# Optimization experiments

Hardware: AMD Instinct MI355X
Metric: run time of the kernel (lower is better)

The kernel has to match this reference:

```python
import jax, jax.numpy as jnp
import numpy as np

C, M, G = 16, 64, 16            # hidden states, alphabet, n_gen
T, D = 64, 10                   # number of trees, depth (perfect binary)
N1 = 2 ** (D + 1) - 1           # nodes per tree (heap layout)
DIM = T * N1                    # total nodes = 131008
N_LEAVES = T * 2 ** D
_E = [T * 2 ** l for l in range(1, D + 1)]        # edges at each level l
_U = [T * 2 ** (l - 1) for l in range(1, D + 1)]  # unique parents at each level l
_EOFF = [0] + list(np.cumsum(_E))
_UOFF = [0] + list(np.cumsum(_U))


def _tree_structure():
    base = (np.arange(T) * N1)[:, None]
    pas, chs, ups = [], [], []
    for l in range(1, D + 1):
        ch = (np.arange(2 ** l - 1, 2 ** (l + 1) - 1)[None, :] + base).reshape(-1)
        pa = (ch % N1 - 1) // 2 + (ch // N1) * N1   # heap parent, global index
        up = (np.arange(2 ** (l - 1) - 1, 2 ** l - 1)[None, :] + base).reshape(-1)
        pas.append(pa); chs.append(ch); ups.append(up)
    return np.concatenate(pas), np.concatenate(chs), np.concatenate(ups)


def setup_inputs() -> dict:
    key = jax.random.key(0)
    k1, k2, k3, k4 = jax.random.split(key, 4)
    pa, ch, up = _tree_structure()
    leaves = (np.arange(2 ** D - 1, N1)[None, :] + (np.arange(T) * N1)[:, None]).reshape(-1)
    return {
        'x': jax.random.randint(k1, (DIM,), 0, M, dtype=jnp.int32),
        'leaves': jnp.asarray(leaves, jnp.int32),
        'trees_ind': jnp.asarray(np.repeat(np.arange(T), N1), jnp.int32),
        'parents_flat': jnp.asarray(pa, jnp.int32),
        'children_flat': jnp.asarray(ch, jnp.int32),
        'uparents_flat': jnp.asarray(up, jnp.int32),
        'inv_map': jnp.arange(DIM, dtype=jnp.int32),
        'lambda_A': jax.random.uniform(k2, (C, C, G), jnp.float32),
        'lambda_B': jax.random.uniform(k3, (C, M, G), jnp.float32),
        'lambda_Pi': jax.random.uniform(k4, (C, G), jnp.float32),
    }


def reference(x, leaves, trees_ind, parents_flat, children_flat, uparents_flat, inv_map,
              lambda_A, lambda_B, lambda_Pi):
    # softmax-normalized parameters (per generative model g)
    A = jax.nn.softmax(lambda_A, axis=0)    # (C,C,G)  transition, normalized over arrival state
    Bm = jax.nn.softmax(lambda_B, axis=1)   # (C,M,G)  emission over symbols
    Pi = jax.nn.softmax(lambda_Pi, axis=0)  # (C,G)    leaf prior

    beta = jnp.zeros((DIM, C, G), lambda_A.dtype)
    ll = jnp.zeros((DIM, G), lambda_A.dtype)

    # leaves: beta = Pi * B[:, x_leaf]
    b_leaf = jnp.transpose(Bm[:, x[inv_map[leaves]]], (1, 0, 2))  # (L,C,G)
    beta_leaf = Pi[None] * b_leaf
    nu = beta_leaf.sum(axis=1)                                    # (L,G)
    beta = beta.at[leaves].set(beta_leaf / nu[:, None, :])
    ll = ll.at[leaves].set(jnp.log(nu))

    # bottom-up over levels (static loop, D=10 iterations)
    for l in range(D, 0, -1):
        e0, e1 = _EOFF[l - 1], _EOFF[l]
        u0, u1 = _UOFF[l - 1], _UOFF[l]
        pa = parents_flat[e0:e1]
        ch = children_flat[e0:e1]
        up = uparents_flat[u0:u1]
        beta_ch = beta[ch]                                   # (E,C,G) gather
        t_beta_ch = jnp.einsum('ijg,ejg->eig', A, beta_ch)   # sum_j A[i,j,g]*beta_ch[e,j,g]
        t_sum = jax.ops.segment_sum(t_beta_ch, pa, num_segments=DIM)
        cnt = jax.ops.segment_sum(jnp.ones((pa.shape[0],), beta.dtype), pa, num_segments=DIM)
        t_beta_up = t_sum[up] / cnt[up][:, None, None]       # scatter-mean over children
        b_l = jnp.transpose(Bm[:, x[inv_map[up]]], (1, 0, 2))
        beta_l = b_l * t_beta_up
        nu = beta_l.sum(axis=1)
        beta = beta.at[up].set(beta_l / nu[:, None, :])
        ll = ll.at[up].set(jnp.log(nu))

    # per-tree log-likelihood: scatter-sum of node log nu over trees
    return jax.ops.segment_sum(ll, trees_ind, num_segments=T)  # (T,G)
```

## Files before the change

### kernel.cpp

```cpp
#include <hip/hip_runtime.h>


#define C_DIM 16
#define M_DIM 64
#define G_DIM 16
#define T_TREES 64
#define N1 2047
#define NBLOCKS (T_TREES * G_DIM)
#define BTS 20

__device__ __forceinline__ float4 f4add(float4 a, float4 b) {
    return make_float4(a.x + b.x, a.y + b.y, a.z + b.z, a.w + b.w);
}
__device__ __forceinline__ float4 f4mul(float4 a, float4 b) {
    return make_float4(a.x * b.x, a.y * b.y, a.z * b.z, a.w * b.w);
}
__device__ __forceinline__ float4 f4fma(float4 a, float4 b, float4 c) {
    return make_float4(fmaf(a.x, b.x, c.x), fmaf(a.y, b.y, c.y),
                       fmaf(a.z, b.z, c.z), fmaf(a.w, b.w, c.w));
}
__device__ __forceinline__ float hsum4(float4 a) { return a.x + a.y + a.z + a.w; }

__device__ __forceinline__ float matvec_bt(const float* __restrict__ A,
                                           const float* __restrict__ bt,
                                           const float4 sv[4], float4 bp[4])
{
    float nu = 0.f;
    #pragma unroll
    for (int h = 0; h < 2; ++h) {
        #pragma unroll
        for (int q = 2 * h; q < 2 * h + 2; ++q) {
            const float4 b4 = *(const float4*)(bt + 4 * q);
            float tr[4];
            #pragma unroll
            for (int r = 0; r < 4; ++r) {
                const float4* ar = (const float4*)(A + (4 * q + r) * 16);
                float4 m = f4mul(ar[0], sv[0]);
                m = f4fma(ar[1], sv[1], m);
                m = f4fma(ar[2], sv[2], m);
                m = f4fma(ar[3], sv[3], m);
                tr[r] = hsum4(m);
            }
            bp[q] = f4mul(make_float4(tr[0], tr[1], tr[2], tr[3]), b4);
            nu += hsum4(bp[q]);
        }
        __builtin_amdgcn_sched_barrier(0);
    }
    return nu;
}

__global__ __launch_bounds__(256, 1) void htmm_fused(
    const int* __restrict__ x,
    const int* __restrict__ inv_map,
    const float* __restrict__ lA,
    const float* __restrict__ lB,
    const float* __restrict__ lPi,
    float* __restrict__ out)
{
    const int bid = blockIdx.x;
    const int tid = threadIdx.x;
    const int g = bid >> 6;
    const int t = bid & (T_TREES - 1);

    __shared__ __align__(16) unsigned char smem[32768];
    float* const sA   = (float*)(smem);
    float* const sBt  = (float*)(smem + 1024);
    float* const sPB  = (float*)(smem + 6144);
    float* const sLog = (float*)(smem + 11264);
    float* const sPi  = (float*)(smem + 11520);
    float* const buf1 = (float*)(smem + 6144);
    unsigned char* const xs = smem + 14336;
    float* const buf0 = (float*)(smem + 16384);
    float* const wsum = (float*)(smem + 32752);

    {
        const int base = t * N1;
        for (int i = tid; i < N1; i += 256)
            xs[i] = (unsigned char)x[inv_map[base + i]];
    }
    {
        int j = tid >> 4, i = tid & 15;
        float v = lA[(i * C_DIM + j) * G_DIM + g];
        float mx = v;
        #pragma unroll
        for (int m = 1; m < 16; m <<= 1) mx = fmaxf(mx, __shfl_xor(mx, m, 16));
        float e = __expf(v - mx);
        float s = e;
        #pragma unroll
        for (int m = 1; m < 16; m <<= 1) s += __shfl_xor(s, m, 16);
        sA[i * C_DIM + j] = e / s;
    }
    {
        int c = tid >> 4, l16 = tid & 15;
        float e0 = lB[(c * M_DIM + l16 +  0) * G_DIM + g];
        float e1 = lB[(c * M_DIM + l16 + 16) * G_DIM + g];
        float e2 = lB[(c * M_DIM + l16 + 32) * G_DIM + g];
        float e3 = lB[(c * M_DIM + l16 + 48) * G_DIM + g];
        float mx = fmaxf(fmaxf(e0, e1), fmaxf(e2, e3));
        #pragma unroll
        for (int m = 1; m < 16; m <<= 1) mx = fmaxf(mx, __shfl_xor(mx, m, 16));
        e0 = __expf(e0 - mx); e1 = __expf(e1 - mx);
        e2 = __expf(e2 - mx); e3 = __expf(e3 - mx);
        float s = e0 + e1 + e2 + e3;
        #pragma unroll
        for (int m = 1; m < 16; m <<= 1) s += __shfl_xor(s, m, 16);
        float inv = 1.f / s;
        sBt[(l16 +  0) * BTS + c] = e0 * inv;
        sBt[(l16 + 16) * BTS + c] = e1 * inv;
        sBt[(l16 + 32) * BTS + c] = e2 * inv;
        sBt[(l16 + 48) * BTS + c] = e3 * inv;
    }
    if (tid < C_DIM) {
        float v = lPi[tid * G_DIM + g];
        float mx = v;
        #pragma unroll
        for (int m = 1; m < 16; m <<= 1) mx = fmaxf(mx, __shfl_xor(mx, m, 16));
        float e = __expf(v - mx);
        float s = e;
        #pragma unroll
        for (int m = 1; m < 16; m <<= 1) s += __shfl_xor(s, m, 16);
        sPi[tid] = e / s;
    }
    __syncthreads();

    if (tid < M_DIM) {
        const int xv = tid;
        float pb[16]; float nu = 0.f;
        #pragma unroll
        for (int k = 0; k < 16; ++k) {
            pb[k] = sPi[k] * sBt[xv * BTS + k];
            nu += pb[k];
        }
        const float inv = 0.5f / nu;
        #pragma unroll
        for (int k = 0; k < 16; ++k) pb[k] *= inv;
        sLog[xv] = __logf(nu);
        const float4 pv0 = make_float4(pb[0],  pb[1],  pb[2],  pb[3]);
        const float4 pv1 = make_float4(pb[4],  pb[5],  pb[6],  pb[7]);
        const float4 pv2 = make_float4(pb[8],  pb[9],  pb[10], pb[11]);
        const float4 pv3 = make_float4(pb[12], pb[13], pb[14], pb[15]);
        float ta[16];
        #pragma unroll
        for (int i = 0; i < 16; ++i) {
            const float4* ar = (const float4*)(sA + i * 16);
            float4 m = f4mul(ar[0], pv0);
            m = f4fma(ar[1], pv1, m);
            m = f4fma(ar[2], pv2, m);
            m = f4fma(ar[3], pv3, m);
            ta[i] = hsum4(m);
            if ((i & 3) == 3) __builtin_amdgcn_sched_barrier(0);
        }
        #pragma unroll
        for (int q = 0; q < 4; ++q)
            *(float4*)(&sPB[xv * BTS + 4 * q]) =
                make_float4(ta[4*q], ta[4*q+1], ta[4*q+2], ta[4*q+3]);
    }
    __syncthreads();

    float ll = 0.f;

    {
        const int idx = tid;
        const int p8  = 255 + idx;
        const int xl0 = xs[4 * p8 + 3], xr0 = xs[4 * p8 + 4];
        const int xl1 = xs[4 * p8 + 5], xr1 = xs[4 * p8 + 6];
        const int xva = xs[2 * p8 + 1], xvb = xs[2 * p8 + 2];
        const int xv8 = xs[p8];

        const float* tl0 = &sPB[xl0 * BTS];
        const float* tr0 = &sPB[xr0 * BTS];
        const float* tl1 = &sPB[xl1 * BTS];
        const float* tr1 = &sPB[xr1 * BTS];
        const float* bta = &sBt[xva * BTS];
        const float* btb = &sBt[xvb * BTS];

        float4 bpa[4], bpb[4];
        float nua = 0.f, nub = 0.f;
        #pragma unroll
        for (int q = 0; q < 4; ++q) {
            float4 tva = f4add(*(const float4*)(tl0 + 4*q),
                               *(const float4*)(tr0 + 4*q));
            float4 tvb = f4add(*(const float4*)(tl1 + 4*q),
                               *(const float4*)(tr1 + 4*q));
            bpa[q] = f4mul(tva, *(const float4*)(bta + 4*q));
            bpb[q] = f4mul(tvb, *(const float4*)(btb + 4*q));
            nua += hsum4(bpa[q]);
            nub += hsum4(bpb[q]);
        }
        const float ia = 0.5f / nua, ib = 0.5f / nub;
        float4 s8v[4];
        #pragma unroll
        for (int q = 0; q < 4; ++q)
            s8v[q] = f4add(f4mul(bpa[q], make_float4(ia, ia, ia, ia)),
                           f4mul(bpb[q], make_float4(ib, ib, ib, ib)));

        float4 bp[4];
        const float nu8 = matvec_bt(sA, &sBt[xv8 * BTS], s8v, bp);
        ll += sLog[xl0] + sLog[xr0] + sLog[xl1] + sLog[xr1]
            + __logf(nua * nub * nu8);
        const float inv = 1.f / nu8;
        #pragma unroll
        for (int q = 0; q < 4; ++q) {
            buf0[(4*q + 0) * 256 + idx] = bp[q].x * inv;
            buf0[(4*q + 1) * 256 + idx] = bp[q].y * inv;
            buf0[(4*q + 2) * 256 + idx] = bp[q].z * inv;
            buf0[(4*q + 3) * 256 + idx] = bp[q].w * inv;
        }
    }
    __syncthreads();

    if (tid < 128) {
        const int idx = tid;
        float4 sv[4];
        #pragma unroll
        for (int q = 0; q < 4; ++q) {
            float2 c0 = *(const float2*)(&buf0[(4*q + 0) * 256 + 2 * idx]);
            float2 c1 = *(const float2*)(&buf0[(4*q + 1) * 256 + 2 * idx]);
            float2 c2 = *(const float2*)(&buf0[(4*q + 2) * 256 + 2 * idx]);
            float2 c3 = *(const float2*)(&buf0[(4*q + 3) * 256 + 2 * idx]);
            sv[q] = make_float4(0.5f * (c0.x + c0.y), 0.5f * (c1.x + c1.y),
                                0.5f * (c2.x + c2.y), 0.5f * (c3.x + c3.y));
        }
        const int xv = xs[127 + idx];
        float4 bp[4];
        float nu = matvec_bt(sA, &sBt[xv * BTS], sv, bp);
        ll += __logf(nu);
        const float inv = 1.f / nu;
        #pragma unroll
        for (int q = 0; q < 4; ++q) {
            buf1[(4*q + 0) * 128 + idx] = bp[q].x * inv;
            buf1[(4*q + 1) * 128 + idx] = bp[q].y * inv;
            buf1[(4*q + 2) * 128 + idx] = bp[q].z * inv;
            buf1[(4*q + 3) * 128 + idx] = bp[q].w * inv;
        }
    }
    __syncthreads();

    if (tid < 64) {
        float* cur = buf1; int cs = 128;
        float* nxt = buf0; int ns = 256;

        {
            const int idx = tid;
            float4 sv[4];
            #pragma unroll
            for (int q = 0; q < 4; ++q) {
                float2 c0 = *(const float2*)(&cur[(4*q + 0) * cs + 2 * idx]);
                float2 c1 = *(const float2*)(&cur[(4*q + 1) * cs + 2 * idx]);
                float2 c2 = *(const float2*)(&cur[(4*q + 2) * cs + 2 * idx]);
                float2 c3 = *(const float2*)(&cur[(4*q + 3) * cs + 2 * idx]);
                sv[q] = make_float4(0.5f * (c0.x + c0.y), 0.5f * (c1.x + c1.y),
                                    0.5f * (c2.x + c2.y), 0.5f * (c3.x + c3.y));
            }
            const int xv = xs[63 + idx];
            float4 bp[4];
            float nu = matvec_bt(sA, &sBt[xv * BTS], sv, bp);
            ll += __logf(nu);
            const float inv = 1.f / nu;
            #pragma unroll
            for (int q = 0; q < 4; ++q) {
                nxt[(4*q + 0) * ns + idx] = bp[q].x * inv;
                nxt[(4*q + 1) * ns + idx] = bp[q].y * inv;
                nxt[(4*q + 2) * ns + idx] = bp[q].z * inv;
                nxt[(4*q + 3) * ns + idx] = bp[q].w * inv;
            }
            asm volatile("s_waitcnt lgkmcnt(0)" ::: "memory");
            __builtin_amdgcn_wave_barrier();
            float* tp = cur; cur = nxt; nxt = tp;
            int ts = cs; cs = ns; ns = ts;
        }

        for (int cnt2 = 32; cnt2 >= 1; cnt2 >>= 1) {
            const int half = tid >> 5;
            const int n    = tid & 31;
            if (n < cnt2) {
                float4 sv[4];
                #pragma unroll
                for (int q = 0; q < 4; ++q) {
                    float2 c0 = *(const float2*)(&cur[(4*q + 0) * cs + 2 * n]);
                    float2 c1 = *(const float2*)(&cur[(4*q + 1) * cs + 2 * n]);
                    float2 c2 = *(const float2*)(&cur[(4*q + 2) * cs + 2 * n]);
                    float2 c3 = *(const float2*)(&cur[(4*q + 3) * cs + 2 * n]);
                    sv[q] = make_float4(0.5f * (c0.x + c0.y), 0.5f * (c1.x + c1.y),
                                        0.5f * (c2.x + c2.y), 0.5f * (c3.x + c3.y));
                }
                const int xv = xs[cnt2 - 1 + n];
                const float* bt = &sBt[xv * BTS];
                const int r0 = half * 8;

                float4 bpA; float hA;
                {
                    float tr[4];
                    #pragma unroll
                    for (int r = 0; r < 4; ++r) {
                        const float4* ar = (const float4*)(sA + (r0 + r) * 16);
                        float4 m = f4mul(ar[0], sv[0]);
                        m = f4fma(ar[1], sv[1], m);
                        m = f4fma(ar[2], sv[2], m);
                        m = f4fma(ar[3], sv[3], m);
                        tr[r] = hsum4(m);
                    }
                    bpA = f4mul(make_float4(tr[0], tr[1], tr[2], tr[3]),
                                *(const float4*)(bt + r0));
                    hA = hsum4(bpA);
                }
                __builtin_amdgcn_sched_barrier(0);
                float4 bpB; float hB;
                {
                    float tr[4];
                    #pragma unroll
                    for (int r = 0; r < 4; ++r) {
                        const float4* ar = (const float4*)(sA + (r0 + 4 + r) * 16);
                        float4 m = f4mul(ar[0], sv[0]);
                        m = f4fma(ar[1], sv[1], m);
                        m = f4fma(ar[2], sv[2], m);
                        m = f4fma(ar[3], sv[3], m);
                        tr[r] = hsum4(m);
                    }
                    bpB = f4mul(make_float4(tr[0], tr[1], tr[2], tr[3]),
                                *(const float4*)(bt + r0 + 4));
                    hB = hsum4(bpB);
                }
                __builtin_amdgcn_sched_barrier(0);

                const float pA = __shfl_xor(hA, 32, 64);
                const float pB = __shfl_xor(hB, 32, 64);
                const float nu = half ? (((pA + pB) + hA) + hB)
                                      : (((hA + hB) + pA) + pB);
                if (half == 0) ll += __logf(nu);
                const float inv = 1.f / nu;
                nxt[(r0 + 0) * ns + n] = bpA.x * inv;
                nxt[(r0 + 1) * ns + n] = bpA.y * inv;
                nxt[(r0 + 2) * ns + n] = bpA.z * inv;
                nxt[(r0 + 3) * ns + n] = bpA.w * inv;
                nxt[(r0 + 4) * ns + n] = bpB.x * inv;
                nxt[(r0 + 5) * ns + n] = bpB.y * inv;
                nxt[(r0 + 6) * ns + n] = bpB.z * inv;
                nxt[(r0 + 7) * ns + n] = bpB.w * inv;
            }
            asm volatile("s_waitcnt lgkmcnt(0)" ::: "memory");
            __builtin_amdgcn_wave_barrier();
            float* tp = cur; cur = nxt; nxt = tp;
            int ts = cs; cs = ns; ns = ts;
        }
    }

    float v = ll;
    #pragma unroll
    for (int off = 32; off > 0; off >>= 1) v += __shfl_down(v, off, 64);
    if ((tid & 63) == 0) wsum[tid >> 6] = v;
    __syncthreads();
    if (tid == 0) out[t * G_DIM + g] = wsum[0] + wsum[1] + wsum[2] + wsum[3];
}

extern "C" void kernel_launch(void* const* d_in, const int* in_sizes, int n_in,
                              void* d_out, int out_size, void* d_ws, size_t ws_size,
                              hipStream_t stream) {
    const int*   x       = (const int*)d_in[0];
    const int*   inv_map = (const int*)d_in[6];
    const float* lA      = (const float*)d_in[7];
    const float* lB      = (const float*)d_in[8];
    const float* lPi     = (const float*)d_in[9];
    float* out = (float*)d_out;

    htmm_fused<<<dim3(NBLOCKS), dim3(256), 0, stream>>>(
        x, inv_map, lA, lB, lPi, out);
}
```

Before: 109.6 us.

## Split upper tree levels across wave halves to use all threads

The 128-node and 64-node levels now use all 256 and 128 threads respectively, with each pair of wave halves computing eight rows of the 16x16 matvec and combining the normaliser through a cross-half shuffle. The single-wave loop starts at the 32-node level, and the shared matvec code is factored into a helper that drops the intermediate sched_barriers. The aim is shorter per-thread serial compute on the upper levels. In exchange it adds shuffles and duplicated normalisation work, and removing the scheduling barriers may change register pressure.

```diff
diff --git a/kernel.cpp b/kernel.cpp
--- a/kernel.cpp
+++ b/kernel.cpp
@@ -49,6 +49,39 @@
     return nu;
 }
 
+__device__ __forceinline__ void halfmv(const float* __restrict__ A,
+                                       const float* __restrict__ bt,
+                                       const float4 sv[4], const int r0,
+                                       float4& bpA, float4& bpB,
+                                       float& hA, float& hB)
+{
+    float trA[4], trB[4];
+    #pragma unroll
+    for (int r = 0; r < 4; ++r) {
+        const float4* ar = (const float4*)(A + (r0 + r) * 16);
+        float4 m = f4mul(ar[0], sv[0]);
+        m = f4fma(ar[1], sv[1], m);
+        m = f4fma(ar[2], sv[2], m);
+        m = f4fma(ar[3], sv[3], m);
+        trA[r] = hsum4(m);
+    }
+    #pragma unroll
+    for (int r = 0; r < 4; ++r) {
+        const float4* ar = (const float4*)(A + (r0 + 4 + r) * 16);
+        float4 m = f4mul(ar[0], sv[0]);
+        m = f4fma(ar[1], sv[1], m);
+        m = f4fma(ar[2], sv[2], m);
+        m = f4fma(ar[3], sv[3], m);
+        trB[r] = hsum4(m);
+    }
+    bpA = f4mul(make_float4(trA[0], trA[1], trA[2], trA[3]),
+                *(const float4*)(bt + r0));
+    bpB = f4mul(make_float4(trB[0], trB[1], trB[2], trB[3]),
+                *(const float4*)(bt + r0 + 4));
+    hA = hsum4(bpA);
+    hB = hsum4(bpB);
+}
+
 __global__ __launch_bounds__(256, 1) void htmm_fused(
     const int* __restrict__ x,
     const int* __restrict__ inv_map,
@@ -209,67 +242,79 @@
     }
     __syncthreads();
 
-    if (tid < 128) {
-        const int idx = tid;
+    {
+        const int w    = tid >> 6;
+        const int half = (tid >> 5) & 1;
+        const int n    = 32 * w + (tid & 31);
         float4 sv[4];
         #pragma unroll
         for (int q = 0; q < 4; ++q) {
-            float2 c0 = *(const float2*)(&buf0[(4*q + 0) * 256 + 2 * idx]);
-            float2 c1 = *(const float2*)(&buf0[(4*q + 1) * 256 + 2 * idx]);
-            float2 c2 = *(const float2*)(&buf0[(4*q + 2) * 256 + 2 * idx]);
-            float2 c3 = *(const float2*)(&buf0[(4*q + 3) * 256 + 2 * idx]);
+            float2 c0 = *(const float2*)(&buf0[(4*q + 0) * 256 + 2 * n]);
+            float2 c1 = *(const float2*)(&buf0[(4*q + 1) * 256 + 2 * n]);
+            float2 c2 = *(const float2*)(&buf0[(4*q + 2) * 256 + 2 * n]);
+            float2 c3 = *(const float2*)(&buf0[(4*q + 3) * 256 + 2 * n]);
             sv[q] = make_float4(0.5f * (c0.x + c0.y), 0.5f * (c1.x + c1.y),
                                 0.5f * (c2.x + c2.y), 0.5f * (c3.x + c3.y));
         }
-        const int xv = xs[127 + idx];
-        float4 bp[4];
-        float nu = matvec_bt(sA, &sBt[xv * BTS], sv, bp);
-        ll += __logf(nu);
+        const int xv = xs[127 + n];
+        const int r0 = half * 8;
+        float4 bpA, bpB; float hA, hB;
+        halfmv(sA, &sBt[xv * BTS], sv, r0, bpA, bpB, hA, hB);
+        const float pA = __shfl_xor(hA, 32, 64);
+        const float pB = __shfl_xor(hB, 32, 64);
+        const float nu = half ? (((pA + pB) + hA) + hB)
+                              : (((hA + hB) + pA) + pB);
+        if (half == 0) ll += __logf(nu);
         const float inv = 1.f / nu;
+        buf1[(r0 + 0) * 128 + n] = bpA.x * inv;
+        buf1[(r0 + 1) * 128 + n] = bpA.y * inv;
+        buf1[(r0 + 2) * 128 + n] = bpA.z * inv;
+        buf1[(r0 + 3) * 128 + n] = bpA.w * inv;
+        buf1[(r0 + 4) * 128 + n] = bpB.x * inv;
+        buf1[(r0 + 5) * 128 + n] = bpB.y * inv;
+        buf1[(r0 + 6) * 128 + n] = bpB.z * inv;
+        buf1[(r0 + 7) * 128 + n] = bpB.w * inv;
+    }
+    __syncthreads();
+
+    if (tid < 128) {
+        const int w    = tid >> 6;
+        const int half = (tid >> 5) & 1;
+        const int n    = 32 * w + (tid & 31);
+        float4 sv[4];
         #pragma unroll
         for (int q = 0; q < 4; ++q) {
-            buf1[(4*q + 0) * 128 + idx] = bp[q].x * inv;
-            buf1[(4*q + 1) * 128 + idx] = bp[q].y * inv;
-            buf1[(4*q + 2) * 128 + idx] = bp[q].z * inv;
-            buf1[(4*q + 3) * 128 + idx] = bp[q].w * inv;
-        }
+            float2 c0 = *(const float2*)(&buf1[(4*q + 0) * 128 + 2 * n]);
+            float2 c1 = *(const float2*)(&buf1[(4*q + 1) * 128 + 2 * n]);
+            float2 c2 = *(const float2*)(&buf1[(4*q + 2) * 128 + 2 * n]);
+            float2 c3 = *(const float2*)(&buf1[(4*q + 3) * 128 + 2 * n]);
+            sv[q] = make_float4(0.5f * (c0.x + c0.y), 0.5f * (c1.x + c1.y),
+                                0.5f * (c2.x + c2.y), 0.5f * (c3.x + c3.y));
+        }
+        const int xv = xs[63 + n];
+        const int r0 = half * 8;
+        float4 bpA, bpB; float hA, hB;
+        halfmv(sA, &sBt[xv * BTS], sv, r0, bpA, bpB, hA, hB);
+        const float pA = __shfl_xor(hA, 32, 64);
+        const float pB = __shfl_xor(hB, 32, 64);
+        const float nu = half ? (((pA + pB) + hA) + hB)
+                              : (((hA + hB) + pA) + pB);
+        if (half == 0) ll += __logf(nu);
+        const float inv = 1.f / nu;
+        buf0[(r0 + 0) * 256 + n] = bpA.x * inv;
+        buf0[(r0 + 1) * 256 + n] = bpA.y * inv;
+        buf0[(r0 + 2) * 256 + n] = bpA.z * inv;
+        buf0[(r0 + 3) * 256 + n] = bpA.w * inv;
+        buf0[(r0 + 4) * 256 + n] = bpB.x * inv;
+        buf0[(r0 + 5) * 256 + n] = bpB.y * inv;
+        buf0[(r0 + 6) * 256 + n] = bpB.z * inv;
+        buf0[(r0 + 7) * 256 + n] = bpB.w * inv;
     }
     __syncthreads();
 
     if (tid < 64) {
-        float* cur = buf1; int cs = 128;
-        float* nxt = buf0; int ns = 256;
-
-        {
-            const int idx = tid;
-            float4 sv[4];
-            #pragma unroll
-            for (int q = 0; q < 4; ++q) {
-                float2 c0 = *(const float2*)(&cur[(4*q + 0) * cs + 2 * idx]);
-                float2 c1 = *(const float2*)(&cur[(4*q + 1) * cs + 2 * idx]);
-                float2 c2 = *(const float2*)(&cur[(4*q + 2) * cs + 2 * idx]);
-                float2 c3 = *(const float2*)(&cur[(4*q + 3) * cs + 2 * idx]);
-                sv[q] = make_float4(0.5f * (c0.x + c0.y), 0.5f * (c1.x + c1.y),
-                                    0.5f * (c2.x + c2.y), 0.5f * (c3.x + c3.y));
-            }
-            const int xv = xs[63 + idx];
-            float4 bp[4];
-            float nu = matvec_bt(sA, &sBt[xv * BTS], sv, bp);
-            ll += __logf(nu);
-            const float inv = 1.f / nu;
-            #pragma unroll
-            for (int q = 0; q < 4; ++q) {
-                nxt[(4*q + 0) * ns + idx] = bp[q].x * inv;
-                nxt[(4*q + 1) * ns + idx] = bp[q].y * inv;
-                nxt[(4*q + 2) * ns + idx] = bp[q].z * inv;
-                nxt[(4*q + 3) * ns + idx] = bp[q].w * inv;
-            }
-            asm volatile("s_waitcnt lgkmcnt(0)" ::: "memory");
-            __builtin_amdgcn_wave_barrier();
-            float* tp = cur; cur = nxt; nxt = tp;
-            int ts = cs; cs = ns; ns = ts;
-        }
-
+        float* cur = buf0; int cs = 256;
+        float* nxt = buf1; int ns = 128;
         for (int cnt2 = 32; cnt2 >= 1; cnt2 >>= 1) {
             const int half = tid >> 5;
             const int n    = tid & 31;
@@ -285,44 +330,9 @@
                                         0.5f * (c2.x + c2.y), 0.5f * (c3.x + c3.y));
                 }
                 const int xv = xs[cnt2 - 1 + n];
-                const float* bt = &sBt[xv * BTS];
                 const int r0 = half * 8;
-
-                float4 bpA; float hA;
-                {
-                    float tr[4];
-                    #pragma unroll
-                    for (int r = 0; r < 4; ++r) {
-                        const float4* ar = (const float4*)(sA + (r0 + r) * 16);
-                        float4 m = f4mul(ar[0], sv[0]);
-                        m = f4fma(ar[1], sv[1], m);
-                        m = f4fma(ar[2], sv[2], m);
-                        m = f4fma(ar[3], sv[3], m);
-                        tr[r] = hsum4(m);
-                    }
-                    bpA = f4mul(make_float4(tr[0], tr[1], tr[2], tr[3]),
-                                *(const float4*)(bt + r0));
-                    hA = hsum4(bpA);
-                }
-                __builtin_amdgcn_sched_barrier(0);
-                float4 bpB; float hB;
-                {
-                    float tr[4];
-                    #pragma unroll
-                    for (int r = 0; r < 4; ++r) {
-                        const float4* ar = (const float4*)(sA + (r0 + 4 + r) * 16);
-                        float4 m = f4mul(ar[0], sv[0]);
-                        m = f4fma(ar[1], sv[1], m);
-                        m = f4fma(ar[2], sv[2], m);
-                        m = f4fma(ar[3], sv[3], m);
-                        tr[r] = hsum4(m);
-                    }
-                    bpB = f4mul(make_float4(tr[0], tr[1], tr[2], tr[3]),
-                                *(const float4*)(bt + r0 + 4));
-                    hB = hsum4(bpB);
-                }
-                __builtin_amdgcn_sched_barrier(0);
-
+                float4 bpA, bpB; float hA, hB;
+                halfmv(sA, &sBt[xv * BTS], sv, r0, bpA, bpB, hA, hB);
                 const float pA = __shfl_xor(hA, 32, 64);
                 const float pB = __shfl_xor(hB, 32, 64);
                 const float nu = half ? (((pA + pB) + hA) + hB)
```

New measurement: 95.16 us. 13.2% less time.
